# Optimization experiments

Hardware: AMD Instinct MI355X
Metric: run time of the kernel (lower is better)

The kernel has to match this reference:

```python
import jax, jax.numpy as jnp
import numpy as np

B, S, D = 8, 1024, 2048          # batch, seq_len, model dim (q_features == kv_features)
H, HD = 16, 128                   # num_heads, head_dim; H*HD == hidden == 2048


def setup_inputs() -> dict:
    key = jax.random.key(0)
    ks = jax.random.split(key, 6)
    fan_in = 1.0 / np.sqrt(D)     # variance_scaling(1.0, 'fan_in') style init scale
    return {
        "inputs_q": jax.random.normal(ks[0], (B, S, D), jnp.float32),
        "inputs_kv": jax.random.normal(ks[1], (B, S, D), jnp.float32),
        "Wq": jax.random.normal(ks[2], (D, H * HD), jnp.float32) * fan_in,
        "Wk": jax.random.normal(ks[3], (D, H * HD), jnp.float32) * fan_in,
        "Wv": jax.random.normal(ks[4], (D, H * HD), jnp.float32) * fan_in,
        "Wo": jax.random.normal(ks[5], (H * HD, D), jnp.float32) * (1.0 / np.sqrt(H * HD)),
    }


def reference(inputs_q, inputs_kv, Wq, Wk, Wv, Wo):
    b, sq, _ = inputs_q.shape
    skv = inputs_kv.shape[1]
    # QKV projections (DenseGeneral, no bias), reshape to heads
    # scale_attn_logits=True -> query scaled by 1/sqrt(head_dim)
    q = (inputs_q @ Wq).reshape(b, sq, H, HD) * (1.0 / np.sqrt(HD))
    k = (inputs_kv @ Wk).reshape(b, skv, H, HD)
    v = (inputs_kv @ Wv).reshape(b, skv, H, HD)
    # dot-product attention core: [b, h, q, k] scores -> softmax -> context
    scores = jnp.einsum('bqhd,bkhd->bhqk', q, k)
    attn = jax.nn.softmax(scores, axis=-1)
    ctx = jnp.einsum('bhqk,bkhd->bqhd', attn, v).reshape(b, sq, H * HD)
    # output projection back to q_features
    return ctx @ Wo
```

## Files before the change

kernel.cpp:

```cpp
#include <hip/hip_runtime.h>
#include <cstdint>
#include <cstddef>

#define B_  8
#define S_  1024
#define D_  2048
#define H_  16
#define HD_ 128
#define NT32_ 64

typedef __bf16 bf16x8 __attribute__((ext_vector_type(8)));
typedef float  f32x4  __attribute__((ext_vector_type(4)));

__device__ __forceinline__ unsigned short f2b(float f) {
    unsigned int u = __float_as_uint(f);
    unsigned int r = (u + 0x7fffu + ((u >> 16) & 1u)) >> 16;
    return (unsigned short)r;
}

__device__ __forceinline__ void gl2lds16(const void* g, void* l) {
    __builtin_amdgcn_global_load_lds(
        (const __attribute__((address_space(1))) void*)g,
        (__attribute__((address_space(3))) void*)l, 16, 0, 0);
}

__global__ void cvt_f32_bf16(const float* __restrict__ src,
                             unsigned short* __restrict__ dst, int n4) {
    int i = blockIdx.x * blockDim.x + threadIdx.x;
    if (i >= n4) return;
    float4 v = ((const float4*)src)[i];
    ushort4 o;
    o.x = f2b(v.x); o.y = f2b(v.y); o.z = f2b(v.z); o.w = f2b(v.w);
    ((ushort4*)dst)[i] = o;
}

__global__ void wtrans(const float* __restrict__ W, unsigned short* __restrict__ Wt) {
    __shared__ float tile[32][33];
    int bx = blockIdx.x, by = blockIdx.y;
    int tx = threadIdx.x, ty = threadIdx.y;
#pragma unroll
    for (int i = 0; i < 4; i++)
        tile[ty + i * 8][tx] = W[(size_t)(by * 32 + ty + i * 8) * D_ + bx * 32 + tx];
    __syncthreads();
#pragma unroll
    for (int i = 0; i < 4; i++)
        Wt[(size_t)(bx * 32 + ty + i * 8) * D_ + by * 32 + tx] = f2b(tile[tx][ty + i * 8]);
}

__global__ void vtrans(const unsigned short* __restrict__ V, unsigned short* __restrict__ Vt) {
    __shared__ unsigned short tile[32][33];
    int bh = blockIdx.z;
    int b = bh >> 4, h = bh & 15;
    int tx = threadIdx.x, ty = threadIdx.y;
    int s0 = blockIdx.x * 32, hd0 = blockIdx.y * 32;
#pragma unroll
    for (int i = 0; i < 4; i++)
        tile[ty + i * 8][tx] = V[(size_t)(b * S_ + s0 + ty + i * 8) * D_ + h * HD_ + hd0 + tx];
    __syncthreads();
#pragma unroll
    for (int i = 0; i < 4; i++)
        Vt[((size_t)bh * HD_ + hd0 + ty + i * 8) * S_ + s0 + tx] = tile[tx][ty + i * 8];
}

#define STAGE(TS, SRC, DST) do {                                                   \
    const int _kb = (TS) * 32;                                                     \
    _Pragma("unroll")                                                              \
    for (int _p = 0; _p < 2; _p++) {                                               \
        int _c = _p * 512 + tid;                                                   \
        int _row = _c >> 2;                                                        \
        int _j = (_c & 3) ^ (_row & 3);                                            \
        gl2lds16(SRC + (size_t)_row * D_ + _kb + _j * 8, DST + _c * 8);            \
    }                                                                              \
} while (0)

#define GTILE(SA, SB, SDA, SDB, TS) do {                                           \
    bf16x8 bF[4], aF[4];                                                           \
    _Pragma("unroll")                                                              \
    for (int j = 0; j < 4; j++)                                                    \
        bF[j] = *(const bf16x8*)(SB + (wn + j * 16 + l15) * 32 + swz);             \
    _Pragma("unroll")                                                              \
    for (int i = 0; i < 4; i++)                                                    \
        aF[i] = *(const bf16x8*)(SA + (wm + i * 16 + l15) * 32 + swz);             \
    STAGE(TS, Ap, SDA);                                                            \
    __builtin_amdgcn_s_barrier();                                                  \
    __builtin_amdgcn_s_setprio(1);                                                 \
    _Pragma("unroll")                                                              \
    for (int i = 0; i < 4; i++)                                                    \
        _Pragma("unroll")                                                          \
        for (int j = 0; j < 4; j++)                                                \
            acc[i][j] = __builtin_amdgcn_mfma_f32_16x16x32_bf16(aF[i], bF[j],      \
                                                               acc[i][j], 0, 0, 0); \
    __builtin_amdgcn_s_setprio(0);                                                 \
    __builtin_amdgcn_s_barrier();                                                  \
    _Pragma("unroll")                                                              \
    for (int i = 0; i < 4; i++)                                                    \
        aF[i] = *(const bf16x8*)(SA + (wm + 64 + i * 16 + l15) * 32 + swz);        \
    STAGE(TS, Bp, SDB);                                                            \
    __builtin_amdgcn_s_barrier();                                                  \
    __builtin_amdgcn_s_setprio(1);                                                 \
    _Pragma("unroll")                                                              \
    for (int i = 0; i < 4; i++)                                                    \
        _Pragma("unroll")                                                          \
        for (int j = 0; j < 4; j++)                                                \
            acc[4 + i][j] = __builtin_amdgcn_mfma_f32_16x16x32_bf16(aF[i], bF[j],  \
                                                               acc[4 + i][j], 0, 0, 0); \
    __builtin_amdgcn_s_setprio(0);                                                 \
    asm volatile("s_waitcnt vmcnt(8)");                                            \
    __builtin_amdgcn_sched_barrier(0);                                             \
    __builtin_amdgcn_s_barrier();                                                  \
} while (0)

template <bool OUTF>
__global__ void __launch_bounds__(512, 2)
gemm_bt4(const unsigned short* __restrict__ A0, const unsigned short* __restrict__ A1,
         const unsigned short* __restrict__ A2,
         const unsigned short* __restrict__ B0, const unsigned short* __restrict__ B1,
         const unsigned short* __restrict__ B2,
         unsigned short* __restrict__ o0, unsigned short* __restrict__ o1,
         unsigned short* __restrict__ o2, float* __restrict__ oF,
         float s0, float s1, float s2) {
    __shared__ __align__(16) unsigned short sA0[256 * 32], sA1[256 * 32];
    __shared__ __align__(16) unsigned short sA2[256 * 32], sA3[256 * 32];
    __shared__ __align__(16) unsigned short sB0[256 * 32], sB1[256 * 32];
    __shared__ __align__(16) unsigned short sB2[256 * 32], sB3[256 * 32];

    const int tid = threadIdx.x;
    const int w = tid >> 6, lane = tid & 63;
    const int l15 = lane & 15, lhi = lane >> 4;

    const int nwgx = gridDim.x;
    const int nwg = nwgx * gridDim.y;
    const int lin = blockIdx.y * nwgx + blockIdx.x;
    const int per = nwg >> 3;
    const int sw = (lin & 7) * per + (lin >> 3);
    const int bx = sw % nwgx, by = sw / nwgx;

    const int region = bx >> 3;
    const unsigned short* A  = region == 0 ? A0 : (region == 1 ? A1 : A2);
    const unsigned short* Bt = region == 0 ? B0 : (region == 1 ? B1 : B2);
    unsigned short* outB     = region == 0 ? o0 : (region == 1 ? o1 : o2);
    const float scale        = region == 0 ? s0 : (region == 1 ? s1 : s2);
    const int mBase = by * 256;
    const int nBase = (bx & 7) * 256;
    const int wm = (w >> 2) * 128, wn = (w & 3) * 64;

    const unsigned short* Ap = A  + (size_t)mBase * D_;
    const unsigned short* Bp = Bt + (size_t)nBase * D_;

    const int swz = (lhi ^ (l15 & 3)) * 8;

    f32x4 acc[8][4] = {};

    STAGE(0, Ap, sA0); STAGE(0, Bp, sB0);
    STAGE(1, Ap, sA1); STAGE(1, Bp, sB1);
    STAGE(2, Ap, sA2); STAGE(2, Bp, sB2);
    asm volatile("s_waitcnt vmcnt(8)");
    __builtin_amdgcn_sched_barrier(0);
    __builtin_amdgcn_s_barrier();

#pragma unroll 1
    for (int tt = 0; tt < NT32_; tt += 4) {
        GTILE(sA0, sB0, sA3, sB3, (tt + 3) & (NT32_ - 1));
        GTILE(sA1, sB1, sA0, sB0, (tt + 4) & (NT32_ - 1));
        GTILE(sA2, sB2, sA1, sB1, (tt + 5) & (NT32_ - 1));
        GTILE(sA3, sB3, sA2, sB2, (tt + 6) & (NT32_ - 1));
    }

    asm volatile("s_waitcnt vmcnt(0)");
    __builtin_amdgcn_sched_barrier(0);
    __builtin_amdgcn_s_barrier();

#pragma unroll
    for (int ai = 0; ai < 8; ai++) {
#pragma unroll
        for (int j = 0; j < 4; j++) {
#pragma unroll
            for (int r = 0; r < 4; r++) {
                int row = mBase + wm + ai * 16 + lhi * 4 + r;
                int col = nBase + wn + j * 16 + l15;
                float v = acc[ai][j][r] * scale;
                if (OUTF) oF[(size_t)row * D_ + col] = v;
                else      outB[(size_t)row * D_ + col] = f2b(v);
            }
        }
    }
}

#define PSTR 72
__global__ void __launch_bounds__(256, 2)
attn(const unsigned short* __restrict__ Q,
     const unsigned short* __restrict__ Kb,
     const unsigned short* __restrict__ Vt,
     unsigned short* __restrict__ ctx) {
    __shared__ unsigned short sK[64 * 128];
    __shared__ unsigned short sV[128 * 64];
    __shared__ unsigned short sP[4 * 32 * PSTR];
    const int tid = threadIdx.x;
    const int w = tid >> 6, lane = tid & 63;
    const int l15 = lane & 15, lhi = lane >> 4;
    const int qt = blockIdx.x, h = blockIdx.y, b = blockIdx.z;
    const unsigned short* Qp = Q  + (size_t)b * S_ * D_ + h * HD_;
    const unsigned short* Kp = Kb + (size_t)b * S_ * D_ + h * HD_;
    const unsigned short* Vp = Vt + (size_t)(b * H_ + h) * HD_ * S_;
    const int q0 = qt * 128 + w * 32;

    int xoff[2];
#pragma unroll
    for (int ks = 0; ks < 2; ks++)
        xoff[ks] = (((ks * 4 + lhi) ^ (l15 & 7)) * 8);

    bf16x8 qF[2][4];
#pragma unroll
    for (int i = 0; i < 2; i++)
#pragma unroll
        for (int kk = 0; kk < 4; kk++)
            qF[i][kk] = *(const bf16x8*)(Qp + (size_t)(q0 + i * 16 + l15) * D_ + kk * 32 + lhi * 8);

    f32x4 o4[2][8] = {};
    float lrun[2][4] = {};
    unsigned short* sPw = sP + w * 32 * PSTR;

    for (int kt = 0; kt < S_ / 64; kt++) {
        __syncthreads();
#pragma unroll
        for (int p = 0; p < 4; p++) {
            int c = p * 256 + tid;
            {
                int row = c >> 4, pc = c & 15;
                int j = pc ^ (row & 7);
                gl2lds16(Kp + (size_t)(kt * 64 + row) * D_ + j * 8, sK + c * 8);
            }
            {
                int row = c >> 3, pc = c & 7;
                int j = pc ^ (row & 7);
                gl2lds16(Vp + (size_t)row * S_ + kt * 64 + j * 8, sV + c * 8);
            }
        }
        __syncthreads();

        f32x4 s4[2][4] = {};
#pragma unroll
        for (int j = 0; j < 4; j++) {
#pragma unroll
            for (int kk = 0; kk < 4; kk++) {
                bf16x8 bFk = *(const bf16x8*)(sK + (j * 16 + l15) * 128 + ((kk * 4 + lhi) ^ (l15 & 7)) * 8);
#pragma unroll
                for (int i = 0; i < 2; i++)
                    s4[i][j] = __builtin_amdgcn_mfma_f32_16x16x32_bf16(qF[i][kk], bFk, s4[i][j], 0, 0, 0);
            }
        }

#pragma unroll
        for (int i = 0; i < 2; i++) {
#pragma unroll
            for (int r = 0; r < 4; r++) {
                int prow = i * 16 + lhi * 4 + r;
                float ps = 0.f;
#pragma unroll
                for (int j = 0; j < 4; j++) {
                    float pv = exp2f(s4[i][j][r]);
                    ps += pv;
                    sPw[prow * PSTR + j * 16 + l15] = f2b(pv);
                }
                lrun[i][r] += ps;
            }
        }

#pragma unroll
        for (int k2 = 0; k2 < 2; k2++) {
            bf16x8 pF[2];
#pragma unroll
            for (int i = 0; i < 2; i++)
                pF[i] = *(const bf16x8*)(sPw + (i * 16 + l15) * PSTR + k2 * 32 + lhi * 8);
#pragma unroll
            for (int nt = 0; nt < 8; nt++) {
                bf16x8 vF = *(const bf16x8*)(sV + (nt * 16 + l15) * 64 + xoff[k2]);
#pragma unroll
                for (int i = 0; i < 2; i++)
                    o4[i][nt] = __builtin_amdgcn_mfma_f32_16x16x32_bf16(pF[i], vF, o4[i][nt], 0, 0, 0);
            }
        }
    }

#pragma unroll
    for (int i = 0; i < 2; i++)
#pragma unroll
        for (int r = 0; r < 4; r++) {
            float s = lrun[i][r];
#pragma unroll
            for (int msk = 1; msk < 16; msk <<= 1) s += __shfl_xor(s, msk);
            lrun[i][r] = 1.0f / s;
        }
#pragma unroll
    for (int i = 0; i < 2; i++)
#pragma unroll
        for (int nt = 0; nt < 8; nt++)
#pragma unroll
            for (int r = 0; r < 4; r++) {
                size_t row = (size_t)b * S_ + q0 + i * 16 + lhi * 4 + r;
                ctx[row * D_ + h * HD_ + nt * 16 + l15] = f2b(o4[i][nt][r] * lrun[i][r]);
            }
}

extern "C" void kernel_launch(void* const* d_in, const int* in_sizes, int n_in,
                              void* d_out, int out_size, void* d_ws, size_t ws_size,
                              hipStream_t stream) {
    const float* Xq  = (const float*)d_in[0];
    const float* Xkv = (const float*)d_in[1];
    const float* Wq  = (const float*)d_in[2];
    const float* Wk  = (const float*)d_in[3];
    const float* Wv  = (const float*)d_in[4];
    const float* Wo  = (const float*)d_in[5];
    float* out = (float*)d_out;

    char* ws = (char*)d_ws;
    const size_t XSZ = (size_t)B_ * S_ * D_ * 2;
    const size_t WSZ = (size_t)D_ * D_ * 2;
    unsigned short* XqB  = (unsigned short*)(ws);
    unsigned short* XkvB = (unsigned short*)(ws + XSZ);
    unsigned short* WqT  = (unsigned short*)(ws + 2 * XSZ);
    unsigned short* WkT  = (unsigned short*)(ws + 2 * XSZ + WSZ);
    unsigned short* WvT  = (unsigned short*)(ws + 2 * XSZ + 2 * WSZ);
    unsigned short* WoT  = (unsigned short*)(ws + 2 * XSZ + 3 * WSZ);
    unsigned short* Qb   = (unsigned short*)(ws + 3 * XSZ);
    unsigned short* Kb   = (unsigned short*)(ws + 4 * XSZ);
    unsigned short* Vb   = (unsigned short*)(ws + 5 * XSZ);
    unsigned short* VtB  = XkvB;
    unsigned short* ctxB = XqB;

    const int n4 = B_ * S_ * D_ / 4;
    cvt_f32_bf16<<<n4 / 256, 256, 0, stream>>>(Xq,  XqB,  n4);
    cvt_f32_bf16<<<n4 / 256, 256, 0, stream>>>(Xkv, XkvB, n4);

    dim3 tb(32, 8);
    wtrans<<<dim3(64, 64), tb, 0, stream>>>(Wq, WqT);
    wtrans<<<dim3(64, 64), tb, 0, stream>>>(Wk, WkT);
    wtrans<<<dim3(64, 64), tb, 0, stream>>>(Wv, WvT);
    wtrans<<<dim3(64, 64), tb, 0, stream>>>(Wo, WoT);

    const float qscale = 1.44269504088896f / 11.313708498984761f;

    gemm_bt4<false><<<dim3(24, 32), 512, 0, stream>>>(
        XqB, XkvB, XkvB, WqT, WkT, WvT, Qb, Kb, Vb, nullptr, qscale, 1.0f, 1.0f);

    vtrans<<<dim3(S_ / 32, HD_ / 32, B_ * H_), tb, 0, stream>>>(Vb, VtB);

    attn<<<dim3(S_ / 128, H_, B_), 256, 0, stream>>>(Qb, Kb, VtB, ctxB);

    gemm_bt4<true><<<dim3(8, 32), 512, 0, stream>>>(
        ctxB, ctxB, ctxB, WoT, WoT, WoT, nullptr, nullptr, nullptr, out, 1.0f, 1.0f, 1.0f);
}
```

Baseline: 639.4 us.

## Restructure GEMM to 256x128 tiles with 4 waves and triple-buffered LDS

```diff
diff --git a/kernel.cpp b/kernel.cpp
--- a/kernel.cpp
+++ b/kernel.cpp
@@ -62,67 +62,63 @@
         Vt[((size_t)bh * HD_ + hd0 + ty + i * 8) * S_ + s0 + tx] = tile[tx][ty + i * 8];
 }
 
-#define STAGE(TS, SRC, DST) do {                                                   \
+#define STAGEA(TS, SRC, DST) do {                                                  \
     const int _kb = (TS) * 32;                                                     \
     _Pragma("unroll")                                                              \
-    for (int _p = 0; _p < 2; _p++) {                                               \
-        int _c = _p * 512 + tid;                                                   \
+    for (int _p = 0; _p < 4; _p++) {                                               \
+        int _c = _p * 256 + tid;                                                   \
         int _row = _c >> 2;                                                        \
-        int _j = (_c & 3) ^ (_row & 3);                                            \
+        int _j = (_c & 3) ^ ((_row >> 1) & 3);                                     \
         gl2lds16(SRC + (size_t)_row * D_ + _kb + _j * 8, DST + _c * 8);            \
     }                                                                              \
 } while (0)
 
-#define GTILE(SA, SB, SDA, SDB, TS) do {                                           \
-    bf16x8 bF[4], aF[4];                                                           \
+#define STAGEB(TS, SRC, DST) do {                                                  \
+    const int _kb = (TS) * 32;                                                     \
+    _Pragma("unroll")                                                              \
+    for (int _p = 0; _p < 2; _p++) {                                               \
+        int _c = _p * 256 + tid;                                                   \
+        int _row = _c >> 2;                                                        \
+        int _j = (_c & 3) ^ ((_row >> 1) & 3);                                     \
+        gl2lds16(SRC + (size_t)_row * D_ + _kb + _j * 8, DST + _c * 8);            \
+    }                                                                              \
+} while (0)
+
+#define KSTEP(SA, SB, SDA, SDB, TS) do {                                           \
+    bf16x8 bF[4], aF[8];                                                           \
     _Pragma("unroll")                                                              \
     for (int j = 0; j < 4; j++)                                                    \
         bF[j] = *(const bf16x8*)(SB + (wn + j * 16 + l15) * 32 + swz);             \
     _Pragma("unroll")                                                              \
-    for (int i = 0; i < 4; i++)                                                    \
+    for (int i = 0; i < 8; i++)                                                    \
         aF[i] = *(const bf16x8*)(SA + (wm + i * 16 + l15) * 32 + swz);             \
-    STAGE(TS, Ap, SDA);                                                            \
-    __builtin_amdgcn_s_barrier();                                                  \
+    STAGEA((TS) & (NT32_ - 1), Ap, SDA);                                           \
+    STAGEB((TS) & (NT32_ - 1), Bp, SDB);                                           \
     __builtin_amdgcn_s_setprio(1);                                                 \
     _Pragma("unroll")                                                              \
-    for (int i = 0; i < 4; i++)                                                    \
+    for (int i = 0; i < 8; i++)                                                    \
         _Pragma("unroll")                                                          \
         for (int j = 0; j < 4; j++)                                                \
             acc[i][j] = __builtin_amdgcn_mfma_f32_16x16x32_bf16(aF[i], bF[j],      \
                                                                acc[i][j], 0, 0, 0); \
     __builtin_amdgcn_s_setprio(0);                                                 \
-    __builtin_amdgcn_s_barrier();                                                  \
-    _Pragma("unroll")                                                              \
-    for (int i = 0; i < 4; i++)                                                    \
-        aF[i] = *(const bf16x8*)(SA + (wm + 64 + i * 16 + l15) * 32 + swz);        \
-    STAGE(TS, Bp, SDB);                                                            \
-    __builtin_amdgcn_s_barrier();                                                  \
-    __builtin_amdgcn_s_setprio(1);                                                 \
-    _Pragma("unroll")                                                              \
-    for (int i = 0; i < 4; i++)                                                    \
-        _Pragma("unroll")                                                          \
-        for (int j = 0; j < 4; j++)                                                \
-            acc[4 + i][j] = __builtin_amdgcn_mfma_f32_16x16x32_bf16(aF[i], bF[j],  \
-                                                               acc[4 + i][j], 0, 0, 0); \
-    __builtin_amdgcn_s_setprio(0);                                                 \
-    asm volatile("s_waitcnt vmcnt(8)");                                            \
+    asm volatile("s_waitcnt vmcnt(6)");                                            \
     __builtin_amdgcn_sched_barrier(0);                                             \
     __builtin_amdgcn_s_barrier();                                                  \
+    __builtin_amdgcn_sched_barrier(0);                                             \
 } while (0)
 
 template <bool OUTF>
-__global__ void __launch_bounds__(512, 2)
-gemm_bt4(const unsigned short* __restrict__ A0, const unsigned short* __restrict__ A1,
+__global__ void __launch_bounds__(256, 2)
+gemm_bt5(const unsigned short* __restrict__ A0, const unsigned short* __restrict__ A1,
          const unsigned short* __restrict__ A2,
          const unsigned short* __restrict__ B0, const unsigned short* __restrict__ B1,
          const unsigned short* __restrict__ B2,
          unsigned short* __restrict__ o0, unsigned short* __restrict__ o1,
          unsigned short* __restrict__ o2, float* __restrict__ oF,
          float s0, float s1, float s2) {
-    __shared__ __align__(16) unsigned short sA0[256 * 32], sA1[256 * 32];
-    __shared__ __align__(16) unsigned short sA2[256 * 32], sA3[256 * 32];
-    __shared__ __align__(16) unsigned short sB0[256 * 32], sB1[256 * 32];
-    __shared__ __align__(16) unsigned short sB2[256 * 32], sB3[256 * 32];
+    __shared__ __align__(16) unsigned short sA0[256 * 32], sA1[256 * 32], sA2[256 * 32];
+    __shared__ __align__(16) unsigned short sB0[128 * 32], sB1[128 * 32], sB2[128 * 32];
 
     const int tid = threadIdx.x;
     const int w = tid >> 6, lane = tid & 63;
@@ -135,35 +131,35 @@
     const int sw = (lin & 7) * per + (lin >> 3);
     const int bx = sw % nwgx, by = sw / nwgx;
 
-    const int region = bx >> 3;
+    const int region = bx >> 4;
     const unsigned short* A  = region == 0 ? A0 : (region == 1 ? A1 : A2);
     const unsigned short* Bt = region == 0 ? B0 : (region == 1 ? B1 : B2);
     unsigned short* outB     = region == 0 ? o0 : (region == 1 ? o1 : o2);
     const float scale        = region == 0 ? s0 : (region == 1 ? s1 : s2);
     const int mBase = by * 256;
-    const int nBase = (bx & 7) * 256;
-    const int wm = (w >> 2) * 128, wn = (w & 3) * 64;
+    const int nBase = (bx & 15) * 128;
+    const int wm = (w >> 1) * 128, wn = (w & 1) * 64;
 
     const unsigned short* Ap = A  + (size_t)mBase * D_;
     const unsigned short* Bp = Bt + (size_t)nBase * D_;
 
-    const int swz = (lhi ^ (l15 & 3)) * 8;
+    const int swz = (lhi ^ ((l15 >> 1) & 3)) * 8;
 
     f32x4 acc[8][4] = {};
 
-    STAGE(0, Ap, sA0); STAGE(0, Bp, sB0);
-    STAGE(1, Ap, sA1); STAGE(1, Bp, sB1);
-    STAGE(2, Ap, sA2); STAGE(2, Bp, sB2);
-    asm volatile("s_waitcnt vmcnt(8)");
+    STAGEA(0, Ap, sA0); STAGEB(0, Bp, sB0);
+    STAGEA(1, Ap, sA1); STAGEB(1, Bp, sB1);
+    asm volatile("s_waitcnt vmcnt(6)");
     __builtin_amdgcn_sched_barrier(0);
     __builtin_amdgcn_s_barrier();
-
+    __builtin_amdgcn_sched_barrier(0);
+
+    KSTEP(sA0, sB0, sA2, sB2, 2);
 #pragma unroll 1
-    for (int tt = 0; tt < NT32_; tt += 4) {
-        GTILE(sA0, sB0, sA3, sB3, (tt + 3) & (NT32_ - 1));
-        GTILE(sA1, sB1, sA0, sB0, (tt + 4) & (NT32_ - 1));
-        GTILE(sA2, sB2, sA1, sB1, (tt + 5) & (NT32_ - 1));
-        GTILE(sA3, sB3, sA2, sB2, (tt + 6) & (NT32_ - 1));
+    for (int tt = 1; tt < NT32_; tt += 3) {
+        KSTEP(sA1, sB1, sA0, sB0, tt + 2);
+        KSTEP(sA2, sB2, sA1, sB1, tt + 3);
+        KSTEP(sA0, sB0, sA2, sB2, tt + 4);
     }
 
     asm volatile("s_waitcnt vmcnt(0)");
@@ -340,13 +336,13 @@
 
     const float qscale = 1.44269504088896f / 11.313708498984761f;
 
-    gemm_bt4<false><<<dim3(24, 32), 512, 0, stream>>>(
+    gemm_bt5<false><<<dim3(48, 32), 256, 0, stream>>>(
         XqB, XkvB, XkvB, WqT, WkT, WvT, Qb, Kb, Vb, nullptr, qscale, 1.0f, 1.0f);
 
     vtrans<<<dim3(S_ / 32, HD_ / 32, B_ * H_), tb, 0, stream>>>(Vb, VtB);
 
     attn<<<dim3(S_ / 128, H_, B_), 256, 0, stream>>>(Qb, Kb, VtB, ctxB);
 
-    gemm_bt4<true><<<dim3(8, 32), 512, 0, stream>>>(
+    gemm_bt5<true><<<dim3(16, 32), 256, 0, stream>>>(
         ctxB, ctxB, ctxB, WoT, WoT, WoT, nullptr, nullptr, nullptr, out, 1.0f, 1.0f, 1.0f);
 }
```

After: 632.5 us. No clear change (-1.1%).
